# Performance work log

Measured on AMD Instinct MI355X. Metric: run time of the kernel, lower is better.

## Reference

```python
import jax, jax.numpy as jnp
import numpy as np

N = 32768          # total nodes
B = 64             # number of graphs (batch.max()+1)
IN_C = 256
OUT_C = 256
NUM_SCALES = 4
NUM_HEADS = 8
BN_EPS = 1e-5


def setup_inputs() -> dict:
    key = jax.random.key(0)
    ks = jax.random.split(key, 10)
    out_s = OUT_C // NUM_SCALES
    x = jax.random.normal(ks[0], (N, IN_C), jnp.float32)
    spectral = jax.random.normal(ks[1], (NUM_SCALES, N, IN_C), jnp.float32)
    batch = jnp.sort(jax.random.randint(ks[2], (N,), 0, B)).astype(jnp.int64)
    # per-scale Linear weights (glorot) and zero biases; stored as [S, in, out_s]
    g = (6.0 / (IN_C + out_s)) ** 0.5
    Ws = jax.random.uniform(ks[3], (NUM_SCALES, IN_C, out_s), jnp.float32, -g, g)
    bs = jnp.zeros((NUM_SCALES, out_s), jnp.float32)
    # MultiheadAttention params (torch layout: in_proj [3E,E], out_proj [E,E])
    s_in = (1.0 / OUT_C) ** 0.5
    W_in = jax.random.uniform(ks[4], (3 * OUT_C, OUT_C), jnp.float32, -s_in, s_in)
    b_in = jnp.zeros((3 * OUT_C,), jnp.float32)
    W_out = jax.random.uniform(ks[5], (OUT_C, OUT_C), jnp.float32, -s_in, s_in)
    b_out = jnp.zeros((OUT_C,), jnp.float32)
    gamma = jnp.ones((OUT_C,), jnp.float32)
    beta = jnp.zeros((OUT_C,), jnp.float32)
    return {"x": x, "spectral": spectral, "Ws": Ws, "bs": bs,
            "W_in": W_in, "b_in": b_in, "W_out": W_out, "b_out": b_out,
            "gamma": gamma, "beta": beta, "batch": batch}


def _forward(x, spectral, Ws, bs, W_in, b_in, W_out, b_out, gamma, beta, batch):
    n, E = x.shape[0], W_out.shape[0]
    # per-scale linear on (x + spectral_feat), concat over scales -> [N, E]
    scale_out = jnp.einsum('sni,sio->sno', x[None] + spectral, Ws) + bs[:, None, :]
    h = jnp.moveaxis(scale_out, 0, 1).reshape(n, E)
    # ragged -> dense padding (batch is sorted segment ids)
    counts = jnp.bincount(batch, length=B)
    max_nodes = int(np.asarray(counts).max())  # data-dependent pad, as in torch
    starts = jnp.concatenate([jnp.zeros((1,), counts.dtype), jnp.cumsum(counts)[:-1]])
    pos = jnp.arange(n) - starts[batch]
    h_pad = jnp.zeros((B, max_nodes, E), h.dtype).at[batch, pos].set(h)
    # MHA over padded graphs (no key-padding mask, matching the source)
    hd = E // NUM_HEADS
    qkv = h_pad @ W_in.T + b_in                       # [B, M, 3E]
    q, k, v = jnp.split(qkv, 3, axis=-1)
    def heads(t):
        return t.reshape(B, max_nodes, NUM_HEADS, hd).transpose(0, 2, 1, 3)
    q, k, v = heads(q) * (hd ** -0.5), heads(k), heads(v)
    attn = jax.nn.softmax(jnp.einsum('bhqd,bhkd->bhqk', q, k), axis=-1)
    ctx = jnp.einsum('bhqk,bhkd->bhqd', attn, v)
    ctx = ctx.transpose(0, 2, 1, 3).reshape(B, max_nodes, E)
    h_att = ctx @ W_out.T + b_out
    # dense -> ragged unpad
    h2 = h_att[batch, pos]                            # [N, E]
    # BatchNorm1d (training-mode batch stats, deterministic) + ReLU; dropout=eval
    mean = h2.mean(axis=0)
    var = h2.var(axis=0)
    hn = (h2 - mean) * jax.lax.rsqrt(var + BN_EPS) * gamma + beta
    return jax.nn.relu(hn)


def reference(x, spectral, Ws, bs, W_in, b_in, W_out, b_out, gamma, beta, batch):
    return _forward(x, spectral, Ws, bs, W_in, b_in, W_out, b_out, gamma, beta, batch)
```

## Files before the change

### kernel.cpp

```cpp
#include <hip/hip_runtime.h>


typedef __attribute__((ext_vector_type(8))) short frag8;
typedef __attribute__((ext_vector_type(4))) short frag4;
typedef __attribute__((ext_vector_type(4))) float f32x4;
typedef __attribute__((ext_vector_type(8))) unsigned short ushort8;
typedef __attribute__((ext_vector_type(2))) unsigned int uint2e;

#define NN 32768
#define NB 64
#define CIN 256
#define COUT 256
#define NHEAD 8
#define HD 32

#define BM 128
#define LDB 264
#define KT 128

#if __has_builtin(__builtin_amdgcn_mfma_f32_16x16x16bf16_1k)
#define HAS_MFMA16 1
#else
#define HAS_MFMA16 0
#endif

#if __has_builtin(__builtin_amdgcn_exp2f)
#define EXP2(x) __builtin_amdgcn_exp2f(x)
#else
#define EXP2(x) __expf((x) * 0.6931471805599453f)
#endif

__device__ inline unsigned short f2bf(float f) {
  unsigned u = __builtin_bit_cast(unsigned, f);
  u += 0x7FFFu + ((u >> 16) & 1u);
  return (unsigned short)(u >> 16);
}
__device__ inline float bf2f(unsigned short h) {
  return __builtin_bit_cast(float, (unsigned)h << 16);
}
__device__ inline unsigned cvtpk(float a, float b) {
  unsigned r;
  asm("v_cvt_pk_bf16_f32 %0, %1, %2" : "=v"(r) : "v"(a), "v"(b));
  return r;
}

__global__ void k_prep(const float* __restrict__ Ws, const float* __restrict__ Win,
                       const float* __restrict__ Wout, const int* __restrict__ batch,
                       unsigned short* __restrict__ wst, unsigned short* __restrict__ winb,
                       unsigned short* __restrict__ woutb, int* __restrict__ meta) {
  int tid = blockIdx.x * 256 + threadIdx.x;
  if (tid < NN) {
    int v = batch[tid];
    int prev = (tid == 0) ? -1 : batch[tid - 1];
    for (int bb = prev + 1; bb <= v; ++bb) meta[NB + bb] = tid;
  }
  if (tid < 4 * 64 * 256) {
    int s = tid >> 14, rem = tid & 16383, o = rem >> 8, i = rem & 255;
    wst[tid] = f2bf(Ws[((s * 256) + i) * 64 + o]);
  } else if (tid < 4 * 64 * 256 + 768 * 256) {
    int t2 = tid - 4 * 64 * 256;
    winb[t2] = f2bf(Win[t2]);
  } else if (tid < 4 * 64 * 256 + 768 * 256 + 256 * 256) {
    int t3 = tid - (4 * 64 * 256 + 768 * 256);
    woutb[t3] = f2bf(Wout[t3]);
  }
}
__global__ void k_meta2(int* __restrict__ meta) {
  __shared__ int mx[NB];
  int b = threadIdx.x;
  int s = meta[NB + b];
  int e = (b == 63) ? NN : meta[NB + b + 1];
  meta[b] = e - s;
  mx[b] = e - s;
  __syncthreads();
  if (b == 0) {
    int m = 0;
    for (int j = 0; j < NB; ++j) m = max(m, mx[j]);
    meta[2 * NB] = m;
  }
}

__device__ inline void stage_Bpanel(const unsigned short* __restrict__ Wt,
                                    unsigned short (*Bs)[LDB], int t) {
  int n = t >> 2, seg = t & 3;
  const unsigned short* src = Wt + (size_t)n * 256 + seg * 64;
#pragma unroll
  for (int i = 0; i < 8; ++i) {
    uint4 v = *(const uint4*)(src + i * 8);
    *(uint4*)&Bs[n][seg * 64 + i * 8] = v;
  }
}


__global__ __launch_bounds__(256, 4) void k_scale(const float* __restrict__ x,
                                                  const float* __restrict__ spec,
                                                  const unsigned short* __restrict__ wst,
                                                  const float* __restrict__ bs,
                                                  unsigned short* __restrict__ h) {
  __shared__ unsigned short Bs[64][LDB];
  int t = threadIdx.x, lane = t & 63, wave = t >> 6;
  int r0 = blockIdx.x * BM, s = blockIdx.y;
  int m16 = lane & 15, quad = lane >> 4;

  stage_Bpanel(wst + (size_t)s * 64 * 256, Bs, t);

  const float* sb = spec + (size_t)s * NN * CIN;
  size_t rowbase0 = (size_t)(r0 + wave * 32 + m16) * CIN + quad * 8;
  size_t rowbase1 = rowbase0 + 16 * CIN;

  float4 P[3][4];
#define ISSUE(slot, kc, mi)                                              \
  do {                                                                   \
    size_t base_ = ((mi) ? rowbase1 : rowbase0) + (size_t)(kc) * 32;     \
    P[(slot)][0] = *(const float4*)(x + base_);                          \
    P[(slot)][1] = *(const float4*)(x + base_ + 4);                      \
    P[(slot)][2] = *(const float4*)(sb + base_);                         \
    P[(slot)][3] = *(const float4*)(sb + base_ + 4);                     \
  } while (0)

  ISSUE(0, 0, 0);
  ISSUE(1, 0, 1);
  ISSUE(2, 1, 0);

  __syncthreads();

  f32x4 z = {0.f, 0.f, 0.f, 0.f};
  f32x4 acc[2][4];
#pragma unroll
  for (int mi = 0; mi < 2; ++mi)
#pragma unroll
    for (int ni = 0; ni < 4; ++ni) acc[mi][ni] = z;

#pragma unroll
  for (int st = 0; st < 16; ++st) {
    const int kc = st >> 1, mi = st & 1, slot = st % 3;
    uint4 u;
    u.x = cvtpk(P[slot][0].x + P[slot][2].x, P[slot][0].y + P[slot][2].y);
    u.y = cvtpk(P[slot][0].z + P[slot][2].z, P[slot][0].w + P[slot][2].w);
    u.z = cvtpk(P[slot][1].x + P[slot][3].x, P[slot][1].y + P[slot][3].y);
    u.w = cvtpk(P[slot][1].z + P[slot][3].z, P[slot][1].w + P[slot][3].w);
    frag8 a = __builtin_bit_cast(frag8, u);
    if (st + 3 < 16) ISSUE(slot, (st + 3) >> 1, (st + 3) & 1);
    frag8 b0 = *(const frag8*)&Bs[m16][kc * 32 + quad * 8];
    frag8 b1 = *(const frag8*)&Bs[16 + m16][kc * 32 + quad * 8];
    frag8 b2 = *(const frag8*)&Bs[32 + m16][kc * 32 + quad * 8];
    frag8 b3 = *(const frag8*)&Bs[48 + m16][kc * 32 + quad * 8];
    acc[mi][0] = __builtin_amdgcn_mfma_f32_16x16x32_bf16(a, b0, acc[mi][0], 0, 0, 0);
    acc[mi][1] = __builtin_amdgcn_mfma_f32_16x16x32_bf16(a, b1, acc[mi][1], 0, 0, 0);
    acc[mi][2] = __builtin_amdgcn_mfma_f32_16x16x32_bf16(a, b2, acc[mi][2], 0, 0, 0);
    acc[mi][3] = __builtin_amdgcn_mfma_f32_16x16x32_bf16(a, b3, acc[mi][3], 0, 0, 0);
  }
#undef ISSUE

#pragma unroll
  for (int mi = 0; mi < 2; ++mi)
#pragma unroll
    for (int ni = 0; ni < 4; ++ni) {
      int col = ni * 16 + m16;
      float bias = bs[s * 64 + col];
#pragma unroll
      for (int rp = 0; rp < 2; ++rp) {
        int row = r0 + wave * 32 + mi * 16 + quad * 4 + rp * 2;
        unsigned u = cvtpk(acc[mi][ni][rp * 2] + bias, acc[mi][ni][rp * 2 + 1] + bias);
        h[(size_t)row * COUT + s * 64 + col] = (unsigned short)u;
        h[(size_t)(row + 1) * COUT + s * 64 + col] = (unsigned short)(u >> 16);
      }
    }
}

template <int LDOUT>
__global__ __launch_bounds__(256, 4) void k_lin(const unsigned short* __restrict__ A,
                                                const unsigned short* __restrict__ Wt,
                                                const float* __restrict__ bias,
                                                unsigned short* __restrict__ out) {
  __shared__ unsigned short Bs[64][LDB];
  int t = threadIdx.x, lane = t & 63, wave = t >> 6;
  int r0 = blockIdx.x * BM, c0 = blockIdx.y * 64;
  int m16 = lane & 15, quad = lane >> 4;

  stage_Bpanel(Wt + (size_t)c0 * 256, Bs, t);

  size_t abase0 = (size_t)(r0 + wave * 32 + m16) * 256 + quad * 8;
  size_t abase1 = abase0 + 16 * 256;

  frag8 PA[3];
  PA[0] = *(const frag8*)(A + abase0);
  PA[1] = *(const frag8*)(A + abase1);
  PA[2] = *(const frag8*)(A + abase0 + 32);

  __syncthreads();

  f32x4 z = {0.f, 0.f, 0.f, 0.f};
  f32x4 acc[2][4];
#pragma unroll
  for (int mi = 0; mi < 2; ++mi)
#pragma unroll
    for (int ni = 0; ni < 4; ++ni) acc[mi][ni] = z;

#pragma unroll
  for (int st = 0; st < 16; ++st) {
    const int kc = st >> 1, mi = st & 1, slot = st % 3;
    frag8 a = PA[slot];
    if (st + 3 < 16) {
      const int nst = st + 3;
      PA[slot] = *(const frag8*)(A + ((nst & 1) ? abase1 : abase0) + (size_t)(nst >> 1) * 32);
    }
    frag8 b0 = *(const frag8*)&Bs[m16][kc * 32 + quad * 8];
    frag8 b1 = *(const frag8*)&Bs[16 + m16][kc * 32 + quad * 8];
    frag8 b2 = *(const frag8*)&Bs[32 + m16][kc * 32 + quad * 8];
    frag8 b3 = *(const frag8*)&Bs[48 + m16][kc * 32 + quad * 8];
    acc[mi][0] = __builtin_amdgcn_mfma_f32_16x16x32_bf16(a, b0, acc[mi][0], 0, 0, 0);
    acc[mi][1] = __builtin_amdgcn_mfma_f32_16x16x32_bf16(a, b1, acc[mi][1], 0, 0, 0);
    acc[mi][2] = __builtin_amdgcn_mfma_f32_16x16x32_bf16(a, b2, acc[mi][2], 0, 0, 0);
    acc[mi][3] = __builtin_amdgcn_mfma_f32_16x16x32_bf16(a, b3, acc[mi][3], 0, 0, 0);
  }

#pragma unroll
  for (int mi = 0; mi < 2; ++mi)
#pragma unroll
    for (int ni = 0; ni < 4; ++ni) {
      int col = c0 + ni * 16 + m16;
      float bv = bias[col];
#pragma unroll
      for (int rp = 0; rp < 2; ++rp) {
        int row = r0 + wave * 32 + mi * 16 + quad * 4 + rp * 2;
        unsigned u = cvtpk(acc[mi][ni][rp * 2] + bv, acc[mi][ni][rp * 2 + 1] + bv);
        out[(size_t)row * LDOUT + col] = (unsigned short)u;
        out[(size_t)(row + 1) * LDOUT + col] = (unsigned short)(u >> 16);
      }
    }
}

__global__ __launch_bounds__(256) void k_attn_mfma(const unsigned short* __restrict__ qkv,
                                                   const int* __restrict__ meta,
                                                   unsigned short* __restrict__ ctx) {
  int b = blockIdx.x >> 3, head = blockIdx.x & 7;
  int c = meta[b], st = meta[NB + b], M = meta[2 * NB];
  int q0 = blockIdx.y * 128;
  if (q0 >= c) return;

  __shared__ unsigned short Vt[32][KT + 8];

  int t = threadIdx.x, lane = t & 63, wave = t >> 6;
  int m16 = lane & 15, quad = lane >> 4;
  const float SC2 = 0.17677669529663687f * 1.4426950408889634f;
  float extra = (float)(M - c);

  int qbase = q0 + wave * 32;
  frag8 qf[2];
#pragma unroll
  for (int qg = 0; qg < 2; ++qg) {
    int qrow = qbase + qg * 16 + m16;
    qf[qg] = *(const frag8*)(qkv + (size_t)(st + qrow) * 768 + head * 32 + quad * 8);
  }

  f32x4 zz = {0.f, 0.f, 0.f, 0.f};
  f32x4 O[2][2];
  float lp[2] = {0.f, 0.f};
#pragma unroll
  for (int qg = 0; qg < 2; ++qg) { O[qg][0] = zz; O[qg][1] = zz; }

#if !HAS_MFMA16
  int sl0 = m16 + ((quad & 1) << 5);
  int sl1 = sl0 + 16;
#endif

  for (int kt = 0; kt < c; kt += KT) {
    {
      int key = t >> 1, dh0 = (t & 1) * 16;
      const unsigned short* vp = qkv + (size_t)(st + kt + key) * 768 + 512 + head * 32 + dh0;
      ushort8 v0 = *(const ushort8*)vp;
      ushort8 v1 = *(const ushort8*)(vp + 8);
#pragma unroll
      for (int i = 0; i < 8; ++i) {
        Vt[dh0 + i][key] = v0[i];
        Vt[dh0 + 8 + i][key] = v1[i];
      }
    }
    __syncthreads();

#pragma unroll
    for (int sub = 0; sub < 4; ++sub) {
      int ks = kt + sub * 32;
      if (ks < c) {
        bool full = (ks + 32 <= c);
        frag8 kf[2];
#pragma unroll
        for (int kh = 0; kh < 2; ++kh) {
          int krow = ks + kh * 16 + m16;
          kf[kh] = *(const frag8*)(qkv + (size_t)(st + krow) * 768 + 256 + head * 32 + quad * 8);
        }
        unsigned pk[2][2][2];
#pragma unroll
        for (int qg = 0; qg < 2; ++qg)
#pragma unroll
          for (int kh = 0; kh < 2; ++kh) {
            f32x4 s = __builtin_amdgcn_mfma_f32_16x16x32_bf16(kf[kh], qf[qg], zz, 0, 0, 0);
            float p[4];
#pragma unroll
            for (int r = 0; r < 4; ++r) p[r] = EXP2(s[r] * SC2);
            if (!full) {
#pragma unroll
              for (int r = 0; r < 4; ++r)
                if (ks + kh * 16 + quad * 4 + r >= c) p[r] = 0.f;
            }
            lp[qg] += (p[0] + p[1]) + (p[2] + p[3]);
            pk[qg][kh][0] = cvtpk(p[0], p[1]);
            pk[qg][kh][1] = cvtpk(p[2], p[3]);
          }
#if HAS_MFMA16
        frag4 vb[2][2];
#pragma unroll
        for (int kh = 0; kh < 2; ++kh)
#pragma unroll
          for (int dh = 0; dh < 2; ++dh)
            vb[kh][dh] = *(const frag4*)&Vt[dh * 16 + m16][sub * 32 + kh * 16 + quad * 4];
#pragma unroll
        for (int qg = 0; qg < 2; ++qg) {
          frag4 pa0 = __builtin_bit_cast(frag4, uint2e{pk[qg][0][0], pk[qg][0][1]});
          frag4 pa1 = __builtin_bit_cast(frag4, uint2e{pk[qg][1][0], pk[qg][1][1]});
#pragma unroll
          for (int dh = 0; dh < 2; ++dh) {
            O[qg][dh] = __builtin_amdgcn_mfma_f32_16x16x16bf16_1k(pa0, vb[0][dh], O[qg][dh], 0, 0, 0);
            O[qg][dh] = __builtin_amdgcn_mfma_f32_16x16x16bf16_1k(pa1, vb[1][dh], O[qg][dh], 0, 0, 0);
          }
        }
#else
        frag8 vf[2];
#pragma unroll
        for (int dh = 0; dh < 2; ++dh)
          vf[dh] = *(const frag8*)&Vt[dh * 16 + m16][sub * 32 + quad * 8];
#pragma unroll
        for (int qg = 0; qg < 2; ++qg) {
          unsigned a0 = __shfl(pk[qg][0][0], sl0), a1 = __shfl(pk[qg][0][1], sl0);
          unsigned a2 = __shfl(pk[qg][0][0], sl1), a3 = __shfl(pk[qg][0][1], sl1);
          unsigned b0 = __shfl(pk[qg][1][0], sl0), b1 = __shfl(pk[qg][1][1], sl0);
          unsigned b2 = __shfl(pk[qg][1][0], sl1), b3 = __shfl(pk[qg][1][1], sl1);
          uint4 pw;
          pw.x = (quad < 2) ? a0 : b0;
          pw.y = (quad < 2) ? a1 : b1;
          pw.z = (quad < 2) ? a2 : b2;
          pw.w = (quad < 2) ? a3 : b3;
          frag8 pf = __builtin_bit_cast(frag8, pw);
#pragma unroll
          for (int dh = 0; dh < 2; ++dh)
            O[qg][dh] = __builtin_amdgcn_mfma_f32_16x16x32_bf16(pf, vf[dh], O[qg][dh], 0, 0, 0);
        }
#endif
      }
    }
    __syncthreads();
  }

#pragma unroll
  for (int qg = 0; qg < 2; ++qg) {
    float v = lp[qg];
    v += __shfl_xor(v, 16);
    v += __shfl_xor(v, 32);
    lp[qg] = v;
  }

#pragma unroll
  for (int qg = 0; qg < 2; ++qg)
#pragma unroll
    for (int r = 0; r < 4; ++r) {
      int qrow = qbase + qg * 16 + quad * 4 + r;
      float lsum = __shfl(lp[qg], quad * 4 + r);
      if (qrow < c) {
        float inv = 1.f / (lsum + extra);
        unsigned short* op = ctx + (size_t)(st + qrow) * 256 + head * 32;
        unsigned u = cvtpk(O[qg][0][r] * inv, O[qg][1][r] * inv);
        op[m16] = (unsigned short)u;
        op[16 + m16] = (unsigned short)(u >> 16);
      }
    }
}

__global__ __launch_bounds__(256) void k_stats(const unsigned short* __restrict__ h,
                                               float* __restrict__ sums) {
  int c = threadIdx.x;
  int r0 = blockIdx.x * 64;
  float s = 0.f, s2 = 0.f;
#pragma unroll 8
  for (int r = 0; r < 64; ++r) {
    float v = bf2f(h[(size_t)(r0 + r) * 256 + c]);
    s += v; s2 += v * v;
  }
  atomicAdd(&sums[c], s);
  atomicAdd(&sums[256 + c], s2);
}

__global__ __launch_bounds__(256) void k_bn_apply(const unsigned short* __restrict__ h,
                                                  const float* __restrict__ sums,
                                                  const float* __restrict__ gamma,
                                                  const float* __restrict__ beta,
                                                  float* __restrict__ out) {
  size_t i8 = ((size_t)blockIdx.x * 256 + threadIdx.x) * 8;
  int c0 = (int)(i8 & 255);
  ushort8 v = *(const ushort8*)(h + i8);
  float4 o0, o1;
  float res[8];
#pragma unroll
  for (int i = 0; i < 8; ++i) {
    int ch = c0 + i;
    float mean = sums[ch] * (1.0f / NN);
    float var = sums[256 + ch] * (1.0f / NN) - mean * mean;
    float sc = rsqrtf(var + 1e-5f) * gamma[ch];
    float sh = beta[ch] - mean * sc;
    res[i] = fmaxf(bf2f(v[i]) * sc + sh, 0.f);
  }
  o0.x = res[0]; o0.y = res[1]; o0.z = res[2]; o0.w = res[3];
  o1.x = res[4]; o1.y = res[5]; o1.z = res[6]; o1.w = res[7];
  *(float4*)(out + i8) = o0;
  *(float4*)(out + i8 + 4) = o1;
}

extern "C" void kernel_launch(void* const* d_in, const int* in_sizes, int n_in,
                              void* d_out, int out_size, void* d_ws, size_t ws_size,
                              hipStream_t stream) {
  const float* x      = (const float*)d_in[0];
  const float* spec   = (const float*)d_in[1];
  const float* Ws     = (const float*)d_in[2];
  const float* bs     = (const float*)d_in[3];
  const float* Win    = (const float*)d_in[4];
  const float* b_in   = (const float*)d_in[5];
  const float* Wout   = (const float*)d_in[6];
  const float* b_out  = (const float*)d_in[7];
  const float* gamma  = (const float*)d_in[8];
  const float* beta   = (const float*)d_in[9];
  const int* batch    = (const int*)d_in[10];
  float* out = (float*)d_out;

  char* w = (char*)d_ws;
  size_t off = 0;
  auto alloc = [&](size_t bytes) -> void* {
    off = (off + 255) & ~(size_t)255;
    void* p = w + off; off += bytes; return p;
  };
  int* meta             = (int*)alloc(129 * sizeof(int));
  unsigned short* wst   = (unsigned short*)alloc((size_t)4 * 64 * 256 * 2);
  unsigned short* winb  = (unsigned short*)alloc((size_t)768 * 256 * 2);
  unsigned short* woutb = (unsigned short*)alloc((size_t)256 * 256 * 2);
  float* sums           = (float*)alloc(512 * 4);
  unsigned short* h     = (unsigned short*)alloc((size_t)NN * 256 * 2);
  unsigned short* qkv   = (unsigned short*)alloc((size_t)NN * 768 * 2);
  unsigned short* ctx   = (unsigned short*)alloc((size_t)NN * 256 * 2);
  unsigned short* hatt  = (unsigned short*)alloc((size_t)NN * 256 * 2);

  (void)hipMemsetAsync(sums, 0, 512 * 4, stream);
  k_prep<<<1280, 256, 0, stream>>>(Ws, Win, Wout, batch, wst, winb, woutb, meta);
  k_meta2<<<1, 64, 0, stream>>>(meta);
  k_scale<<<dim3(NN / BM, 4), 256, 0, stream>>>(x, spec, wst, bs, h);
  k_lin<768><<<dim3(NN / BM, 12), 256, 0, stream>>>(h, winb, b_in, qkv);
  k_attn_mfma<<<dim3(NB * NHEAD, 8), 256, 0, stream>>>(qkv, meta, ctx);
  k_lin<256><<<dim3(NN / BM, 4), 256, 0, stream>>>(ctx, woutb, b_out, hatt);
  k_stats<<<NN / 64, 256, 0, stream>>>(hatt, sums);
  k_bn_apply<<<NN * 256 / 2048, 256, 0, stream>>>(hatt, sums, gamma, beta, out);
}
```

Before: 396.8 us.

## Fuse BN stats into output projection and swizzle block order for XCD locality

Removes the separate column-statistics kernel by accumulating per-column sum and sum-of-squares in the output-projection GEMM epilogue, reduced with shuffles and atomics. Flattens the GEMM and attention grids and remaps block indices so neighbouring row tiles or graphs land on the same XCD, aiming at better L2 reuse. Pointer arithmetic is also simplified. Stats are now computed from fp32 values before bf16 rounding, and the change adds many more atomics.

```diff
diff --git a/kernel.cpp b/kernel.cpp
--- a/kernel.cpp
+++ b/kernel.cpp
@@ -98,24 +98,31 @@
                                                   const float* __restrict__ bs,
                                                   unsigned short* __restrict__ h) {
   __shared__ unsigned short Bs[64][LDB];
+  int bid = blockIdx.x;
+  int bx = (bid & 7) * 32 + ((bid >> 3) & 31);
+  int s = bid >> 8;
   int t = threadIdx.x, lane = t & 63, wave = t >> 6;
-  int r0 = blockIdx.x * BM, s = blockIdx.y;
+  int r0 = bx * BM;
   int m16 = lane & 15, quad = lane >> 4;
 
   stage_Bpanel(wst + (size_t)s * 64 * 256, Bs, t);
 
   const float* sb = spec + (size_t)s * NN * CIN;
   size_t rowbase0 = (size_t)(r0 + wave * 32 + m16) * CIN + quad * 8;
-  size_t rowbase1 = rowbase0 + 16 * CIN;
+  const float* px0 = x + rowbase0;
+  const float* px1 = px0 + 16 * CIN;
+  const float* ps0 = sb + rowbase0;
+  const float* ps1 = ps0 + 16 * CIN;
 
   float4 P[3][4];
 #define ISSUE(slot, kc, mi)                                              \
   do {                                                                   \
-    size_t base_ = ((mi) ? rowbase1 : rowbase0) + (size_t)(kc) * 32;     \
-    P[(slot)][0] = *(const float4*)(x + base_);                          \
-    P[(slot)][1] = *(const float4*)(x + base_ + 4);                      \
-    P[(slot)][2] = *(const float4*)(sb + base_);                         \
-    P[(slot)][3] = *(const float4*)(sb + base_ + 4);                     \
+    const float* px_ = (mi) ? px1 : px0;                                 \
+    const float* ps_ = (mi) ? ps1 : ps0;                                 \
+    P[(slot)][0] = *(const float4*)(px_ + (kc) * 32);                    \
+    P[(slot)][1] = *(const float4*)(px_ + (kc) * 32 + 4);                \
+    P[(slot)][2] = *(const float4*)(ps_ + (kc) * 32);                    \
+    P[(slot)][3] = *(const float4*)(ps_ + (kc) * 32 + 4);                \
   } while (0)
 
   ISSUE(0, 0, 0);
@@ -168,25 +175,29 @@
     }
 }
 
-template <int LDOUT>
+template <int LDOUT, int NCB, bool DOSTATS>
 __global__ __launch_bounds__(256, 4) void k_lin(const unsigned short* __restrict__ A,
                                                 const unsigned short* __restrict__ Wt,
                                                 const float* __restrict__ bias,
-                                                unsigned short* __restrict__ out) {
+                                                unsigned short* __restrict__ out,
+                                                float* __restrict__ sums) {
   __shared__ unsigned short Bs[64][LDB];
+  int bid = blockIdx.x;
+  int bx = (bid & 7) * 32 + ((bid >> 3) & 31);
+  int cb = bid >> 8;
   int t = threadIdx.x, lane = t & 63, wave = t >> 6;
-  int r0 = blockIdx.x * BM, c0 = blockIdx.y * 64;
+  int r0 = bx * BM, c0 = cb * 64;
   int m16 = lane & 15, quad = lane >> 4;
 
   stage_Bpanel(Wt + (size_t)c0 * 256, Bs, t);
 
-  size_t abase0 = (size_t)(r0 + wave * 32 + m16) * 256 + quad * 8;
-  size_t abase1 = abase0 + 16 * 256;
+  const unsigned short* pa0 = A + (size_t)(r0 + wave * 32 + m16) * 256 + quad * 8;
+  const unsigned short* pa1 = pa0 + 16 * 256;
 
   frag8 PA[3];
-  PA[0] = *(const frag8*)(A + abase0);
-  PA[1] = *(const frag8*)(A + abase1);
-  PA[2] = *(const frag8*)(A + abase0 + 32);
+  PA[0] = *(const frag8*)(pa0);
+  PA[1] = *(const frag8*)(pa1);
+  PA[2] = *(const frag8*)(pa0 + 32);
 
   __syncthreads();
 
@@ -203,7 +214,7 @@
     frag8 a = PA[slot];
     if (st + 3 < 16) {
       const int nst = st + 3;
-      PA[slot] = *(const frag8*)(A + ((nst & 1) ? abase1 : abase0) + (size_t)(nst >> 1) * 32);
+      PA[slot] = *(const frag8*)(((nst & 1) ? pa1 : pa0) + (nst >> 1) * 32);
     }
     frag8 b0 = *(const frag8*)&Bs[m16][kc * 32 + quad * 8];
     frag8 b1 = *(const frag8*)&Bs[16 + m16][kc * 32 + quad * 8];
@@ -216,25 +227,40 @@
   }
 
 #pragma unroll
-  for (int mi = 0; mi < 2; ++mi)
-#pragma unroll
-    for (int ni = 0; ni < 4; ++ni) {
-      int col = c0 + ni * 16 + m16;
-      float bv = bias[col];
+  for (int ni = 0; ni < 4; ++ni) {
+    int col = c0 + ni * 16 + m16;
+    float bv = bias[col];
+    float s1 = 0.f, s2 = 0.f;
+#pragma unroll
+    for (int mi = 0; mi < 2; ++mi) {
 #pragma unroll
       for (int rp = 0; rp < 2; ++rp) {
+        float v0 = acc[mi][ni][rp * 2] + bv;
+        float v1 = acc[mi][ni][rp * 2 + 1] + bv;
+        if (DOSTATS) { s1 += v0 + v1; s2 += v0 * v0 + v1 * v1; }
         int row = r0 + wave * 32 + mi * 16 + quad * 4 + rp * 2;
-        unsigned u = cvtpk(acc[mi][ni][rp * 2] + bv, acc[mi][ni][rp * 2 + 1] + bv);
+        unsigned u = cvtpk(v0, v1);
         out[(size_t)row * LDOUT + col] = (unsigned short)u;
         out[(size_t)(row + 1) * LDOUT + col] = (unsigned short)(u >> 16);
       }
     }
+    if (DOSTATS) {
+      s1 += __shfl_xor(s1, 16); s1 += __shfl_xor(s1, 32);
+      s2 += __shfl_xor(s2, 16); s2 += __shfl_xor(s2, 32);
+      if (quad == 0) {
+        atomicAdd(&sums[col], s1);
+        atomicAdd(&sums[256 + col], s2);
+      }
+    }
+  }
 }
 
 __global__ __launch_bounds__(256) void k_attn_mfma(const unsigned short* __restrict__ qkv,
                                                    const int* __restrict__ meta,
                                                    unsigned short* __restrict__ ctx) {
-  int b = blockIdx.x >> 3, head = blockIdx.x & 7;
+  int bidx = blockIdx.x;
+  int b = (bidx & 7) * 8 + ((bidx >> 3) & 7);
+  int head = bidx >> 6;
   int c = meta[b], st = meta[NB + b], M = meta[2 * NB];
   int q0 = blockIdx.y * 128;
   if (q0 >= c) return;
@@ -374,20 +400,6 @@
         op[16 + m16] = (unsigned short)(u >> 16);
       }
     }
-}
-
-__global__ __launch_bounds__(256) void k_stats(const unsigned short* __restrict__ h,
-                                               float* __restrict__ sums) {
-  int c = threadIdx.x;
-  int r0 = blockIdx.x * 64;
-  float s = 0.f, s2 = 0.f;
-#pragma unroll 8
-  for (int r = 0; r < 64; ++r) {
-    float v = bf2f(h[(size_t)(r0 + r) * 256 + c]);
-    s += v; s2 += v * v;
-  }
-  atomicAdd(&sums[c], s);
-  atomicAdd(&sums[256 + c], s2);
 }
 
 __global__ __launch_bounds__(256) void k_bn_apply(const unsigned short* __restrict__ h,
@@ -450,10 +462,9 @@
   (void)hipMemsetAsync(sums, 0, 512 * 4, stream);
   k_prep<<<1280, 256, 0, stream>>>(Ws, Win, Wout, batch, wst, winb, woutb, meta);
   k_meta2<<<1, 64, 0, stream>>>(meta);
-  k_scale<<<dim3(NN / BM, 4), 256, 0, stream>>>(x, spec, wst, bs, h);
-  k_lin<768><<<dim3(NN / BM, 12), 256, 0, stream>>>(h, winb, b_in, qkv);
+  k_scale<<<NN / BM * 4, 256, 0, stream>>>(x, spec, wst, bs, h);
+  k_lin<768, 12, false><<<NN / BM * 12, 256, 0, stream>>>(h, winb, b_in, qkv, nullptr);
   k_attn_mfma<<<dim3(NB * NHEAD, 8), 256, 0, stream>>>(qkv, meta, ctx);
-  k_lin<256><<<dim3(NN / BM, 4), 256, 0, stream>>>(ctx, woutb, b_out, hatt);
-  k_stats<<<NN / 64, 256, 0, stream>>>(hatt, sums);
+  k_lin<256, 4, true><<<NN / BM * 4, 256, 0, stream>>>(ctx, woutb, b_out, hatt, sums);
   k_bn_apply<<<NN * 256 / 2048, 256, 0, stream>>>(hatt, sums, gamma, beta, out);
 }
```

Result: slower. 414.2 us (+4.4%).
